# Kernel tuning notes

Hardware: AMD Instinct MI355X
Metric: run time of the kernel (lower is better)

## Reference

```python
import jax, jax.numpy as jnp
import numpy as np

H = 12
D_K = 64
NEG = -1e9
EPS = 1e-6
SQRT_2_PI = float(np.sqrt(2.0 / np.pi))


def gelu_tanh(x):
    return 0.5 * x * (1.0 + jnp.tanh(SQRT_2_PI * (x + 0.044715 * x * x * x)))


def layernorm(x, a, b):
    # torch std is unbiased (ddof=1); note original adds eps to std, not var
    mean = jnp.mean(x, axis=-1, keepdims=True)
    n = x.shape[-1]
    var = jnp.sum((x - mean) ** 2, axis=-1, keepdims=True) / (n - 1)
    std = jnp.sqrt(var)
    return a * (x - mean) / (std + EPS) + b


def setup_inputs() -> dict:
    key = jax.random.key(0)
    ks = jax.random.split(key, 16)
    B, S, D, F = 8, 1024, 768, 3072
    s = 0.02
    inp = {
        "x": jax.random.normal(ks[0], (B, S, D), jnp.float32),
        "mask": jnp.ones((B, 1, 1, S), jnp.int32),
        "Wq": jax.random.normal(ks[1], (D, D), jnp.float32) * s,
        "bq": jnp.zeros((D,), jnp.float32),
        "Wk": jax.random.normal(ks[2], (D, D), jnp.float32) * s,
        "bk": jnp.zeros((D,), jnp.float32),
        "Wv": jax.random.normal(ks[3], (D, D), jnp.float32) * s,
        "bv": jnp.zeros((D,), jnp.float32),
        "Wo": jax.random.normal(ks[4], (D, D), jnp.float32) * s,
        "bo": jnp.zeros((D,), jnp.float32),
        "W1": jax.random.normal(ks[5], (D, F), jnp.float32) * s,
        "b1": jnp.zeros((F,), jnp.float32),
        "W2": jax.random.normal(ks[6], (F, D), jnp.float32) * s,
        "b2": jnp.zeros((D,), jnp.float32),
        "ln1_a": jnp.ones((D,), jnp.float32),
        "ln1_b": jnp.ones((D,), jnp.float32),
        "ln2_a": jnp.ones((D,), jnp.float32),
        "ln2_b": jnp.ones((D,), jnp.float32),
    }
    return inp


def reference(x, mask, Wq, bq, Wk, bk, Wv, bv, Wo, bo, W1, b1, W2, b2,
              ln1_a, ln1_b, ln2_a, ln2_b):
    B, S, D = x.shape
    # QKV projections -> [B, H, S, d_k]
    def split_heads(t):
        return t.reshape(B, S, H, D_K).transpose(0, 2, 1, 3)
    q = split_heads(x @ Wq + bq)
    k = split_heads(x @ Wk + bk)
    v = split_heads(x @ Wv + bv)
    scores = jnp.einsum("bhqd,bhkd->bhqk", q, k) / jnp.sqrt(jnp.float32(D_K))
    scores = jnp.where(mask == 0, jnp.float32(NEG), scores)
    p = jax.nn.softmax(scores, axis=-1)
    attn = jnp.einsum("bhqk,bhkd->bhqd", p, v)
    attn = attn.transpose(0, 2, 1, 3).reshape(B, S, D)
    attn_out = attn @ Wo + bo
    out1 = layernorm(x + attn_out, ln1_a, ln1_b)
    ffn = gelu_tanh(out1 @ W1 + b1) @ W2 + b2
    out2 = layernorm(out1 + ffn, ln2_a, ln2_b)
    return out2
```

## Files before the change

kernel.cpp:

```cpp
#include <hip/hip_runtime.h>
#include <hip/hip_bf16.h>
#include <math.h>

#define BB 8
#define SS 1024
#define DD 768
#define FF 3072
#define HH 12
#define DK 64

typedef __bf16 bf16;
typedef __attribute__((ext_vector_type(8))) __bf16 bf16x8;
typedef __attribute__((ext_vector_type(4))) __bf16 bf16x4;
typedef __attribute__((ext_vector_type(4))) float f32x4;

#define AS1 __attribute__((address_space(1)))
#define AS3 __attribute__((address_space(3)))

#define EXP2_SCALE 0.18033688011112042f
#define NLOG2E2    -2.8853900817779268f

__device__ __forceinline__ float gelu_fast(float x) {
    const float u = 0.7978845608028654f * (x + 0.044715f * x * x * x);
    const float e = __builtin_amdgcn_exp2f(u * NLOG2E2);
    return x * __builtin_amdgcn_rcpf(1.0f + e);
}

template<int BN, int OUTB, int GELU_F, int RESID>
__global__ __launch_bounds__(256) void gemm_bf16(
    const bf16* __restrict__ A, const bf16* __restrict__ Bt,
    const float* __restrict__ bias, const float* __restrict__ R,
    void* __restrict__ Cout, int M, int N, int K)
{
    constexpr int NTJ   = BN / 32;
    constexpr int BITER = (BN * 8) / 256;

    __shared__ bf16x8 As[1024];
    __shared__ bf16x8 Bs[BN * 8];

    const int t    = threadIdx.x;
    const int wave = t >> 6;
    const int lane = t & 63;
    const int mtiles = M >> 7;
    const int m0 = (blockIdx.x % mtiles) * 128;
    const int n0 = (blockIdx.x / mtiles) * BN;
    const int wm = (wave >> 1) * 64;
    const int wn = (wave & 1) * (BN / 2);
    const int col  = lane & 15;
    const int quad = lane >> 4;

    f32x4 acc[4][NTJ] = {};

    const bf16* Abase = A  + (size_t)m0 * K;
    const bf16* Bbase = Bt + (size_t)n0 * K;

    for (int k0 = 0; k0 < K; k0 += 64) {
        if (k0) __syncthreads();

        #pragma unroll
        for (int i = 0; i < 4; ++i) {
            const int chunk = i * 256 + wave * 64 + lane;
            const int r  = chunk >> 3;
            const int kc = (chunk & 7) ^ (r & 7);
            const bf16* ga = Abase + (size_t)r * K + k0 + kc * 8;
            __builtin_amdgcn_global_load_lds((AS1 void*)ga, (AS3 void*)(As + i * 256 + wave * 64), 16, 0, 0);
        }
        #pragma unroll
        for (int i = 0; i < BITER; ++i) {
            const int chunk = i * 256 + wave * 64 + lane;
            const int r  = chunk >> 3;
            const int kc = (chunk & 7) ^ (r & 7);
            const bf16* gb = Bbase + (size_t)r * K + k0 + kc * 8;
            __builtin_amdgcn_global_load_lds((AS1 void*)gb, (AS3 void*)(Bs + i * 256 + wave * 64), 16, 0, 0);
        }
        __syncthreads();

        const bf16* Asp = (const bf16*)As;
        const bf16* Bsp = (const bf16*)Bs;
        #pragma unroll
        for (int ks = 0; ks < 2; ++ks) {
            bf16x8 af[4], bfr[NTJ];
            #pragma unroll
            for (int ti = 0; ti < 4; ++ti) {
                const int r  = wm + ti * 16 + col;
                const int cs = (ks * 4 + quad) ^ (r & 7);
                af[ti] = *(const bf16x8*)(Asp + r * 64 + cs * 8);
            }
            #pragma unroll
            for (int tj = 0; tj < NTJ; ++tj) {
                const int r  = wn + tj * 16 + col;
                const int cs = (ks * 4 + quad) ^ (r & 7);
                bfr[tj] = *(const bf16x8*)(Bsp + r * 64 + cs * 8);
            }
            #pragma unroll
            for (int ti = 0; ti < 4; ++ti)
                #pragma unroll
                for (int tj = 0; tj < NTJ; ++tj)
                    acc[ti][tj] = __builtin_amdgcn_mfma_f32_16x16x32_bf16(
                        af[ti], bfr[tj], acc[ti][tj], 0, 0, 0);
        }
    }

    float biasv[NTJ];
    #pragma unroll
    for (int tj = 0; tj < NTJ; ++tj) biasv[tj] = bias[n0 + wn + tj * 16 + col];

    #pragma unroll
    for (int ti = 0; ti < 4; ++ti) {
        #pragma unroll
        for (int tj = 0; tj < NTJ; ++tj) {
            const int n = n0 + wn + tj * 16 + col;
            #pragma unroll
            for (int i = 0; i < 4; ++i) {
                const int m = m0 + wm + ti * 16 + quad * 4 + i;
                float v = acc[ti][tj][i] + biasv[tj];
                if (GELU_F) v = gelu_fast(v);
                if (RESID) v += R[(size_t)m * N + n];
                if (OUTB) ((bf16*)Cout)[(size_t)m * N + n] = (bf16)v;
                else      ((float*)Cout)[(size_t)m * N + n] = v;
            }
        }
    }
}

__device__ __forceinline__ void tc32(
    const float* __restrict__ src, bf16* __restrict__ dst,
    int R, int C, int c0, int r0, int t)
{
    __shared__ float tile[32][33];
    const int tx = t & 31, ty = t >> 5;
    #pragma unroll
    for (int i = 0; i < 32; i += 8)
        tile[ty + i][tx] = src[(size_t)(r0 + ty + i) * C + c0 + tx];
    __syncthreads();
    #pragma unroll
    for (int i = 0; i < 32; i += 8)
        dst[(size_t)(c0 + ty + i) * R + r0 + tx] = (bf16)tile[tx][ty + i];
}

__global__ __launch_bounds__(256) void prep_all(
    const float* __restrict__ Wq, const float* __restrict__ Wk,
    const float* __restrict__ Wv, const float* __restrict__ Wo,
    const float* __restrict__ W1, const float* __restrict__ W2,
    const float* __restrict__ bq, const float* __restrict__ bk,
    const float* __restrict__ bv, const float* __restrict__ x,
    bf16* __restrict__ wqkvb, bf16* __restrict__ wob,
    bf16* __restrict__ wt1b,  bf16* __restrict__ wt2b,
    float* __restrict__ bqkv, bf16x4* __restrict__ xb)
{
    const int blk = blockIdx.x;
    const int t = threadIdx.x;
    if (blk < 2304) {
        const int job = blk / 576, loc = blk % 576;
        const int c0 = (loc % 24) * 32, r0 = (loc / 24) * 32;
        const float* src = (job == 0) ? Wq : (job == 1) ? Wk : (job == 2) ? Wv : Wo;
        bf16* dst = (job == 3) ? wob : wqkvb + (size_t)job * DD * DD;
        tc32(src, dst, DD, DD, c0, r0, t);
    } else if (blk < 4608) {
        const int loc = blk - 2304;
        tc32(W1, wt1b, DD, FF, (loc % 96) * 32, (loc / 96) * 32, t);
    } else if (blk < 6912) {
        const int loc = blk - 4608;
        tc32(W2, wt2b, FF, DD, (loc % 24) * 32, (loc / 24) * 32, t);
    } else if (blk < 6921) {
        const int i = (blk - 6912) * 256 + t;
        if (i < 3 * DD)
            bqkv[i] = (i < DD) ? bq[i] : (i < 2 * DD ? bk[i - DD] : bv[i - 2 * DD]);
    } else {
        const int i = (blk - 6921) * 256 + t;
        const float4 v = ((const float4*)x)[i];
        bf16x4 o;
        o.x = (bf16)v.x; o.y = (bf16)v.y; o.z = (bf16)v.z; o.w = (bf16)v.w;
        xb[i] = o;
    }
}

__global__ __launch_bounds__(256) void vtrans(
    const bf16* __restrict__ qkvb, bf16* __restrict__ vtb)
{
    __shared__ bf16 tile[32][33];
    const int s0 = blockIdx.x * 32, d0 = blockIdx.y * 32;
    const int bh = blockIdx.z;
    const int b = bh / HH, h = bh % HH;
    const int tx = threadIdx.x & 31, ty = threadIdx.x >> 5;
    #pragma unroll
    for (int i = 0; i < 32; i += 8)
        tile[ty + i][tx] = qkvb[(size_t)(b * SS + s0 + ty + i) * 2304 + 1536 + h * DK + d0 + tx];
    __syncthreads();
    #pragma unroll
    for (int i = 0; i < 32; i += 8)
        vtb[(size_t)(bh * DK + d0 + ty + i) * SS + s0 + tx] = tile[tx][ty + i];
}

__global__ __launch_bounds__(256) void flash_mfma(
    const bf16* __restrict__ qkvb,
    const bf16* __restrict__ vtb,
    const int*  __restrict__ mask,
    bf16* __restrict__ O)
{
    __shared__ bf16x8 Ks[512];
    __shared__ bf16x8 Vs[512];
    __shared__ bf16   Ps[4 * 32 * 64];

    const int t    = threadIdx.x;
    const int wave = t >> 6;
    const int lane = t & 63;
    const int col  = lane & 15;
    const int quad = lane >> 4;
    const int bh = blockIdx.x % (BB * HH);
    const int q0 = (blockIdx.x / (BB * HH)) * 128;
    const int b  = bh / HH;
    const int h  = bh % HH;

    bf16x8 aq[2][2];
    #pragma unroll
    for (int mi = 0; mi < 2; ++mi)
        #pragma unroll
        for (int ks = 0; ks < 2; ++ks)
            aq[mi][ks] = *(const bf16x8*)(qkvb
                + (size_t)(b * SS + q0 + wave * 32 + mi * 16 + col) * 2304
                + h * DK + ks * 32 + quad * 8);

    f32x4 o[2][4] = {};
    float l_part[2][4] = {};

    bf16* Pw = Ps + wave * 2048;

    for (int c0 = 0; c0 < SS; c0 += 64) {
        if (c0) __syncthreads();

        #pragma unroll
        for (int i = 0; i < 2; ++i) {
            const int s  = i * 256 + wave * 64 + lane;
            const int r  = s >> 3;
            const int kc = (s & 7) ^ (r & 7);
            const bf16* gk = qkvb + (size_t)(b * SS + c0 + r) * 2304 + DD + h * DK + kc * 8;
            __builtin_amdgcn_global_load_lds((AS1 void*)gk, (AS3 void*)(Ks + i * 256 + wave * 64), 16, 0, 0);
            const bf16* gv = vtb + (size_t)(bh * DK + r) * SS + c0 + kc * 8;
            __builtin_amdgcn_global_load_lds((AS1 void*)gv, (AS3 void*)(Vs + i * 256 + wave * 64), 16, 0, 0);
        }
        __syncthreads();

        const bf16* Ksp = (const bf16*)Ks;
        f32x4 s4[2][4] = {};
        {
            bf16x8 kf[2][4];
            #pragma unroll
            for (int ks = 0; ks < 2; ++ks)
                #pragma unroll
                for (int tj = 0; tj < 4; ++tj) {
                    const int r  = tj * 16 + col;
                    const int sl = (ks * 4 + quad) ^ (r & 7);
                    kf[ks][tj] = *(const bf16x8*)(Ksp + r * 64 + sl * 8);
                }
            #pragma unroll
            for (int mi = 0; mi < 2; ++mi)
                #pragma unroll
                for (int ks = 0; ks < 2; ++ks)
                    #pragma unroll
                    for (int tj = 0; tj < 4; ++tj)
                        s4[mi][tj] = __builtin_amdgcn_mfma_f32_16x16x32_bf16(
                            aq[mi][ks], kf[ks][tj], s4[mi][tj], 0, 0, 0);
        }

        int mk[4];
        #pragma unroll
        for (int tj = 0; tj < 4; ++tj) mk[tj] = mask[b * SS + c0 + tj * 16 + col];

        #pragma unroll
        for (int mi = 0; mi < 2; ++mi)
            #pragma unroll
            for (int i = 0; i < 4; ++i) {
                const int rf = mi * 16 + quad * 4 + i;
                #pragma unroll
                for (int tj = 0; tj < 4; ++tj) {
                    const float sv = (mk[tj] == 0) ? -1e9f : s4[mi][tj][i];
                    const float p = __builtin_amdgcn_exp2f(sv * EXP2_SCALE);
                    l_part[mi][i] += p;
                    const int c  = tj * 16 + col;
                    const int sl = ((c >> 3) ^ (rf & 7));
                    Pw[rf * 64 + sl * 8 + (c & 7)] = (bf16)p;
                }
            }

        const bf16* Vsp = (const bf16*)Vs;
        bf16x8 vf[2][4];
        #pragma unroll
        for (int ks = 0; ks < 2; ++ks)
            #pragma unroll
            for (int tj = 0; tj < 4; ++tj) {
                const int r  = tj * 16 + col;
                const int sl = (ks * 4 + quad) ^ (r & 7);
                vf[ks][tj] = *(const bf16x8*)(Vsp + r * 64 + sl * 8);
            }
        #pragma unroll
        for (int mi = 0; mi < 2; ++mi) {
            bf16x8 pf[2];
            #pragma unroll
            for (int ks = 0; ks < 2; ++ks) {
                const int rf = mi * 16 + col;
                const int sl = (ks * 4 + quad) ^ (rf & 7);
                pf[ks] = *(const bf16x8*)(Pw + rf * 64 + sl * 8);
            }
            #pragma unroll
            for (int ks = 0; ks < 2; ++ks)
                #pragma unroll
                for (int tj = 0; tj < 4; ++tj)
                    o[mi][tj] = __builtin_amdgcn_mfma_f32_16x16x32_bf16(
                        pf[ks], vf[ks][tj], o[mi][tj], 0, 0, 0);
        }
    }

    #pragma unroll
    for (int mi = 0; mi < 2; ++mi)
        #pragma unroll
        for (int i = 0; i < 4; ++i) {
            float l = l_part[mi][i];
            #pragma unroll
            for (int off = 1; off < 16; off <<= 1)
                l += __shfl_xor(l, off, 64);
            const float inv = 1.0f / l;
            const int q = q0 + wave * 32 + mi * 16 + quad * 4 + i;
            #pragma unroll
            for (int tj = 0; tj < 4; ++tj)
                O[(size_t)(b * SS + q) * DD + h * DK + tj * 16 + col] =
                    (bf16)(o[mi][tj][i] * inv);
        }
}

__global__ __launch_bounds__(256) void layernorm_k(
    const float* __restrict__ X,
    const float* __restrict__ ga, const float* __restrict__ gb,
    float* __restrict__ out, bf16* __restrict__ outb)
{
    __shared__ float red[4];
    const int row = blockIdx.x;
    const int t   = threadIdx.x;
    const float* x = X + (size_t)row * DD;

    float v[3];
    #pragma unroll
    for (int i = 0; i < 3; ++i) v[i] = x[t + i * 256];

    float s = v[0] + v[1] + v[2];
    #pragma unroll
    for (int off = 32; off > 0; off >>= 1) s += __shfl_down(s, off, 64);
    if ((t & 63) == 0) red[t >> 6] = s;
    __syncthreads();
    const float mean = (red[0] + red[1] + red[2] + red[3]) * (1.0f / 768.0f);
    __syncthreads();

    float sq = 0.f;
    #pragma unroll
    for (int i = 0; i < 3; ++i) { const float d = v[i] - mean; sq += d * d; }
    #pragma unroll
    for (int off = 32; off > 0; off >>= 1) sq += __shfl_down(sq, off, 64);
    if ((t & 63) == 0) red[t >> 6] = sq;
    __syncthreads();
    const float var = (red[0] + red[1] + red[2] + red[3]) * (1.0f / 767.0f);
    const float inv = 1.0f / (sqrtf(var) + 1e-6f);

    #pragma unroll
    for (int i = 0; i < 3; ++i) {
        const int c = t + i * 256;
        const float r = ga[c] * (v[i] - mean) * inv + gb[c];
        out[(size_t)row * DD + c] = r;
        if (outb) outb[(size_t)row * DD + c] = (bf16)r;
    }
}

extern "C" void kernel_launch(void* const* d_in, const int* in_sizes, int n_in,
                              void* d_out, int out_size, void* d_ws, size_t ws_size,
                              hipStream_t stream)
{
    const float* x    = (const float*)d_in[0];
    const int*   mask = (const int*)  d_in[1];
    const float* Wq   = (const float*)d_in[2];
    const float* bq   = (const float*)d_in[3];
    const float* Wk   = (const float*)d_in[4];
    const float* bk   = (const float*)d_in[5];
    const float* Wv   = (const float*)d_in[6];
    const float* bv   = (const float*)d_in[7];
    const float* Wo   = (const float*)d_in[8];
    const float* bo   = (const float*)d_in[9];
    const float* W1   = (const float*)d_in[10];
    const float* b1   = (const float*)d_in[11];
    const float* W2   = (const float*)d_in[12];
    const float* b2   = (const float*)d_in[13];
    const float* ln1a = (const float*)d_in[14];
    const float* ln1b = (const float*)d_in[15];
    const float* ln2a = (const float*)d_in[16];
    const float* ln2b = (const float*)d_in[17];
    float* out = (float*)d_out;

    const int M = BB * SS;
    const size_t nBSD = (size_t)M * DD;

    char* w = (char*)d_ws;
    bf16*  qkvb  = (bf16*)w;            w += (size_t)M * 3 * DD * 2;
    bf16*  vtb   = (bf16*)w;            w += (size_t)BB * HH * DK * SS * 2;
    bf16*  attnb = (bf16*)w;            w += nBSD * 2;
    float* attn_sum = (float*)w;        w += nBSD * 4;
    float* out1  = (float*)w;           w += nBSD * 4;
    float* ffn_sum = (float*)w;         w += nBSD * 4;
    bf16*  xb    = (bf16*)w;            w += nBSD * 2;
    bf16*  hbuf  = (bf16*)w;            w += (size_t)M * FF * 2;
    bf16*  wqkvb = (bf16*)w;            w += (size_t)3 * DD * DD * 2;
    bf16*  wob   = (bf16*)w;            w += (size_t)DD * DD * 2;
    bf16*  wt1b  = (bf16*)w;            w += (size_t)DD * FF * 2;
    bf16*  wt2b  = (bf16*)w;            w += (size_t)FF * DD * 2;
    float* bqkv  = (float*)w;           w += (size_t)3 * DD * 4;
    bf16*  out1b = xb;

    const dim3 blk(256);

    prep_all<<<dim3(13065), blk, 0, stream>>>(
        Wq, Wk, Wv, Wo, W1, W2, bq, bk, bv, x,
        wqkvb, wob, wt1b, wt2b, bqkv, (bf16x4*)xb);

    gemm_bf16<128, 1, 0, 0><<<dim3((M / 128) * (3 * DD / 128)), blk, 0, stream>>>(
        xb, wqkvb, bqkv, nullptr, qkvb, M, 3 * DD, DD);

    vtrans<<<dim3(SS / 32, DK / 32, BB * HH), blk, 0, stream>>>(qkvb, vtb);

    flash_mfma<<<dim3((SS / 128) * BB * HH), blk, 0, stream>>>(qkvb, vtb, mask, attnb);

    gemm_bf16<64, 0, 0, 1><<<dim3((M / 128) * (DD / 64)), blk, 0, stream>>>(
        attnb, wob, bo, x, attn_sum, M, DD, DD);

    layernorm_k<<<dim3(M), blk, 0, stream>>>(attn_sum, ln1a, ln1b, out1, out1b);

    gemm_bf16<128, 1, 1, 0><<<dim3((M / 128) * (FF / 128)), blk, 0, stream>>>(
        out1b, wt1b, b1, nullptr, hbuf, M, FF, DD);

    gemm_bf16<64, 0, 0, 1><<<dim3((M / 128) * (DD / 64)), blk, 0, stream>>>(
        hbuf, wt2b, b2, out1, ffn_sum, M, DD, FF);

    layernorm_k<<<dim3(M), blk, 0, stream>>>(ffn_sum, ln2a, ln2b, out, nullptr);
}
```

Measured before the change: 364.0 us.

## Store residual sums in bf16 and double flash attention key chunk per barrier

The Wo and W2 GEMM outputs (pre-layernorm residual sums) are now written as bf16 instead of fp32. The layernorms read bf16, the first layernorm stops writing its fp32 copy, and the second residual add reads the bf16 out1. Flash attention now loads 128 keys per barrier, processed as two 64-key halves with doubled LDS buffers, and applies the mask as an additive bias folded into an fma. This cuts intermediate memory traffic and barrier count, at the cost of bf16 rounding on residual paths and more LDS per block, which may lower occupancy.

```diff
diff --git a/kernel.cpp b/kernel.cpp
--- a/kernel.cpp
+++ b/kernel.cpp
@@ -19,6 +19,7 @@
 
 #define EXP2_SCALE 0.18033688011112042f
 #define NLOG2E2    -2.8853900817779268f
+#define MASK_BIAS  -1.8e8f
 
 __device__ __forceinline__ float gelu_fast(float x) {
     const float u = 0.7978845608028654f * (x + 0.044715f * x * x * x);
@@ -26,10 +27,10 @@
     return x * __builtin_amdgcn_rcpf(1.0f + e);
 }
 
-template<int BN, int OUTB, int GELU_F, int RESID>
+template<int BN, int OUTB, int GELU_F, int RESID, int RB>
 __global__ __launch_bounds__(256) void gemm_bf16(
     const bf16* __restrict__ A, const bf16* __restrict__ Bt,
-    const float* __restrict__ bias, const float* __restrict__ R,
+    const float* __restrict__ bias, const void* __restrict__ R,
     void* __restrict__ Cout, int M, int N, int K)
 {
     constexpr int NTJ   = BN / 32;
@@ -115,7 +116,11 @@
                 const int m = m0 + wm + ti * 16 + quad * 4 + i;
                 float v = acc[ti][tj][i] + biasv[tj];
                 if (GELU_F) v = gelu_fast(v);
-                if (RESID) v += R[(size_t)m * N + n];
+                if (RESID) {
+                    const size_t idx = (size_t)m * N + n;
+                    v += RB ? (float)((const bf16*)R)[idx]
+                            : ((const float*)R)[idx];
+                }
                 if (OUTB) ((bf16*)Cout)[(size_t)m * N + n] = (bf16)v;
                 else      ((float*)Cout)[(size_t)m * N + n] = v;
             }
@@ -198,8 +203,8 @@
     const int*  __restrict__ mask,
     bf16* __restrict__ O)
 {
-    __shared__ bf16x8 Ks[512];
-    __shared__ bf16x8 Vs[512];
+    __shared__ bf16x8 Ks[1024];
+    __shared__ bf16x8 Vs[1024];
     __shared__ bf16   Ps[4 * 32 * 64];
 
     const int t    = threadIdx.x;
@@ -226,88 +231,105 @@
 
     bf16* Pw = Ps + wave * 2048;
 
-    for (int c0 = 0; c0 < SS; c0 += 64) {
+    for (int c0 = 0; c0 < SS; c0 += 128) {
         if (c0) __syncthreads();
 
         #pragma unroll
-        for (int i = 0; i < 2; ++i) {
-            const int s  = i * 256 + wave * 64 + lane;
-            const int r  = s >> 3;
-            const int kc = (s & 7) ^ (r & 7);
-            const bf16* gk = qkvb + (size_t)(b * SS + c0 + r) * 2304 + DD + h * DK + kc * 8;
-            __builtin_amdgcn_global_load_lds((AS1 void*)gk, (AS3 void*)(Ks + i * 256 + wave * 64), 16, 0, 0);
-            const bf16* gv = vtb + (size_t)(bh * DK + r) * SS + c0 + kc * 8;
-            __builtin_amdgcn_global_load_lds((AS1 void*)gv, (AS3 void*)(Vs + i * 256 + wave * 64), 16, 0, 0);
+        for (int i = 0; i < 4; ++i) {
+            const int chunk = i * 256 + wave * 64 + lane;
+            const int half  = chunk >> 9;
+            const int wi    = chunk & 511;
+            const int r  = wi >> 3;
+            const int kc = (wi & 7) ^ (r & 7);
+            const bf16* gk = qkvb + (size_t)(b * SS + c0 + half * 64 + r) * 2304
+                           + DD + h * DK + kc * 8;
+            __builtin_amdgcn_global_load_lds((AS1 void*)gk, (AS3 void*)(Ks + chunk - lane + lane), 16, 0, 0);
+        }
+        #pragma unroll
+        for (int i = 0; i < 4; ++i) {
+            const int chunk = i * 256 + wave * 64 + lane;
+            const int half  = chunk >> 9;
+            const int wi    = chunk & 511;
+            const int r  = wi >> 3;
+            const int kc = (wi & 7) ^ (r & 7);
+            const bf16* gv = vtb + (size_t)(bh * DK + r) * SS + c0 + half * 64 + kc * 8;
+            __builtin_amdgcn_global_load_lds((AS1 void*)gv, (AS3 void*)(Vs + chunk - lane + lane), 16, 0, 0);
         }
         __syncthreads();
 
-        const bf16* Ksp = (const bf16*)Ks;
-        f32x4 s4[2][4] = {};
-        {
-            bf16x8 kf[2][4];
+        #pragma unroll
+        for (int half = 0; half < 2; ++half) {
+            const bf16* Ksp = (const bf16*)(Ks + half * 512);
+            const bf16* Vsp = (const bf16*)(Vs + half * 512);
+            const int ch0 = c0 + half * 64;
+
+            f32x4 s4[2][4] = {};
+            {
+                bf16x8 kf[2][4];
+                #pragma unroll
+                for (int ks = 0; ks < 2; ++ks)
+                    #pragma unroll
+                    for (int tj = 0; tj < 4; ++tj) {
+                        const int r  = tj * 16 + col;
+                        const int sl = (ks * 4 + quad) ^ (r & 7);
+                        kf[ks][tj] = *(const bf16x8*)(Ksp + r * 64 + sl * 8);
+                    }
+                #pragma unroll
+                for (int mi = 0; mi < 2; ++mi)
+                    #pragma unroll
+                    for (int ks = 0; ks < 2; ++ks)
+                        #pragma unroll
+                        for (int tj = 0; tj < 4; ++tj)
+                            s4[mi][tj] = __builtin_amdgcn_mfma_f32_16x16x32_bf16(
+                                aq[mi][ks], kf[ks][tj], s4[mi][tj], 0, 0, 0);
+            }
+
+            float addb[4];
+            #pragma unroll
+            for (int tj = 0; tj < 4; ++tj)
+                addb[tj] = mask[b * SS + ch0 + tj * 16 + col] ? 0.0f : MASK_BIAS;
+
+            #pragma unroll
+            for (int mi = 0; mi < 2; ++mi)
+                #pragma unroll
+                for (int i = 0; i < 4; ++i) {
+                    const int rf = mi * 16 + quad * 4 + i;
+                    #pragma unroll
+                    for (int tj = 0; tj < 4; ++tj) {
+                        const float p = __builtin_amdgcn_exp2f(
+                            fmaf(s4[mi][tj][i], EXP2_SCALE, addb[tj]));
+                        l_part[mi][i] += p;
+                        const int c  = tj * 16 + col;
+                        const int sl = ((c >> 3) ^ (rf & 7));
+                        Pw[rf * 64 + sl * 8 + (c & 7)] = (bf16)p;
+                    }
+                }
+
+            bf16x8 vf[2][4];
             #pragma unroll
             for (int ks = 0; ks < 2; ++ks)
                 #pragma unroll
                 for (int tj = 0; tj < 4; ++tj) {
                     const int r  = tj * 16 + col;
                     const int sl = (ks * 4 + quad) ^ (r & 7);
-                    kf[ks][tj] = *(const bf16x8*)(Ksp + r * 64 + sl * 8);
+                    vf[ks][tj] = *(const bf16x8*)(Vsp + r * 64 + sl * 8);
                 }
             #pragma unroll
-            for (int mi = 0; mi < 2; ++mi)
+            for (int mi = 0; mi < 2; ++mi) {
+                bf16x8 pf[2];
+                #pragma unroll
+                for (int ks = 0; ks < 2; ++ks) {
+                    const int rf = mi * 16 + col;
+                    const int sl = (ks * 4 + quad) ^ (rf & 7);
+                    pf[ks] = *(const bf16x8*)(Pw + rf * 64 + sl * 8);
+                }
                 #pragma unroll
                 for (int ks = 0; ks < 2; ++ks)
                     #pragma unroll
                     for (int tj = 0; tj < 4; ++tj)
-                        s4[mi][tj] = __builtin_amdgcn_mfma_f32_16x16x32_bf16(
-                            aq[mi][ks], kf[ks][tj], s4[mi][tj], 0, 0, 0);
-        }
-
-        int mk[4];
-        #pragma unroll
-        for (int tj = 0; tj < 4; ++tj) mk[tj] = mask[b * SS + c0 + tj * 16 + col];
-
-        #pragma unroll
-        for (int mi = 0; mi < 2; ++mi)
-            #pragma unroll
-            for (int i = 0; i < 4; ++i) {
-                const int rf = mi * 16 + quad * 4 + i;
-                #pragma unroll
-                for (int tj = 0; tj < 4; ++tj) {
-                    const float sv = (mk[tj] == 0) ? -1e9f : s4[mi][tj][i];
-                    const float p = __builtin_amdgcn_exp2f(sv * EXP2_SCALE);
-                    l_part[mi][i] += p;
-                    const int c  = tj * 16 + col;
-                    const int sl = ((c >> 3) ^ (rf & 7));
-                    Pw[rf * 64 + sl * 8 + (c & 7)] = (bf16)p;
-                }
+                        o[mi][tj] = __builtin_amdgcn_mfma_f32_16x16x32_bf16(
+                            pf[ks], vf[ks][tj], o[mi][tj], 0, 0, 0);
             }
-
-        const bf16* Vsp = (const bf16*)Vs;
-        bf16x8 vf[2][4];
-        #pragma unroll
-        for (int ks = 0; ks < 2; ++ks)
-            #pragma unroll
-            for (int tj = 0; tj < 4; ++tj) {
-                const int r  = tj * 16 + col;
-                const int sl = (ks * 4 + quad) ^ (r & 7);
-                vf[ks][tj] = *(const bf16x8*)(Vsp + r * 64 + sl * 8);
-            }
-        #pragma unroll
-        for (int mi = 0; mi < 2; ++mi) {
-            bf16x8 pf[2];
-            #pragma unroll
-            for (int ks = 0; ks < 2; ++ks) {
-                const int rf = mi * 16 + col;
-                const int sl = (ks * 4 + quad) ^ (rf & 7);
-                pf[ks] = *(const bf16x8*)(Pw + rf * 64 + sl * 8);
-            }
-            #pragma unroll
-            for (int ks = 0; ks < 2; ++ks)
-                #pragma unroll
-                for (int tj = 0; tj < 4; ++tj)
-                    o[mi][tj] = __builtin_amdgcn_mfma_f32_16x16x32_bf16(
-                        pf[ks], vf[ks][tj], o[mi][tj], 0, 0, 0);
         }
     }
 
@@ -329,18 +351,18 @@
 }
 
 __global__ __launch_bounds__(256) void layernorm_k(
-    const float* __restrict__ X,
+    const bf16* __restrict__ X,
     const float* __restrict__ ga, const float* __restrict__ gb,
     float* __restrict__ out, bf16* __restrict__ outb)
 {
     __shared__ float red[4];
     const int row = blockIdx.x;
     const int t   = threadIdx.x;
-    const float* x = X + (size_t)row * DD;
+    const bf16* x = X + (size_t)row * DD;
 
     float v[3];
     #pragma unroll
-    for (int i = 0; i < 3; ++i) v[i] = x[t + i * 256];
+    for (int i = 0; i < 3; ++i) v[i] = (float)x[t + i * 256];
 
     float s = v[0] + v[1] + v[2];
     #pragma unroll
@@ -364,7 +386,7 @@
     for (int i = 0; i < 3; ++i) {
         const int c = t + i * 256;
         const float r = ga[c] * (v[i] - mean) * inv + gb[c];
-        out[(size_t)row * DD + c] = r;
+        if (out)  out[(size_t)row * DD + c] = r;
         if (outb) outb[(size_t)row * DD + c] = (bf16)r;
     }
 }
@@ -400,9 +422,8 @@
     bf16*  qkvb  = (bf16*)w;            w += (size_t)M * 3 * DD * 2;
     bf16*  vtb   = (bf16*)w;            w += (size_t)BB * HH * DK * SS * 2;
     bf16*  attnb = (bf16*)w;            w += nBSD * 2;
-    float* attn_sum = (float*)w;        w += nBSD * 4;
-    float* out1  = (float*)w;           w += nBSD * 4;
-    float* ffn_sum = (float*)w;         w += nBSD * 4;
+    bf16*  attn_sumb = (bf16*)w;        w += nBSD * 2;
+    bf16*  ffn_sumb  = (bf16*)w;        w += nBSD * 2;
     bf16*  xb    = (bf16*)w;            w += nBSD * 2;
     bf16*  hbuf  = (bf16*)w;            w += (size_t)M * FF * 2;
     bf16*  wqkvb = (bf16*)w;            w += (size_t)3 * DD * DD * 2;
@@ -418,23 +439,23 @@
         Wq, Wk, Wv, Wo, W1, W2, bq, bk, bv, x,
         wqkvb, wob, wt1b, wt2b, bqkv, (bf16x4*)xb);
 
-    gemm_bf16<128, 1, 0, 0><<<dim3((M / 128) * (3 * DD / 128)), blk, 0, stream>>>(
+    gemm_bf16<128, 1, 0, 0, 0><<<dim3((M / 128) * (3 * DD / 128)), blk, 0, stream>>>(
         xb, wqkvb, bqkv, nullptr, qkvb, M, 3 * DD, DD);
 
     vtrans<<<dim3(SS / 32, DK / 32, BB * HH), blk, 0, stream>>>(qkvb, vtb);
 
     flash_mfma<<<dim3((SS / 128) * BB * HH), blk, 0, stream>>>(qkvb, vtb, mask, attnb);
 
-    gemm_bf16<64, 0, 0, 1><<<dim3((M / 128) * (DD / 64)), blk, 0, stream>>>(
-        attnb, wob, bo, x, attn_sum, M, DD, DD);
-
-    layernorm_k<<<dim3(M), blk, 0, stream>>>(attn_sum, ln1a, ln1b, out1, out1b);
-
-    gemm_bf16<128, 1, 1, 0><<<dim3((M / 128) * (FF / 128)), blk, 0, stream>>>(
+    gemm_bf16<64, 1, 0, 1, 0><<<dim3((M / 128) * (DD / 64)), blk, 0, stream>>>(
+        attnb, wob, bo, x, attn_sumb, M, DD, DD);
+
+    layernorm_k<<<dim3(M), blk, 0, stream>>>(attn_sumb, ln1a, ln1b, nullptr, out1b);
+
+    gemm_bf16<128, 1, 1, 0, 0><<<dim3((M / 128) * (FF / 128)), blk, 0, stream>>>(
         out1b, wt1b, b1, nullptr, hbuf, M, FF, DD);
 
-    gemm_bf16<64, 0, 0, 1><<<dim3((M / 128) * (DD / 64)), blk, 0, stream>>>(
-        hbuf, wt2b, b2, out1, ffn_sum, M, DD, FF);
-
-    layernorm_k<<<dim3(M), blk, 0, stream>>>(ffn_sum, ln2a, ln2b, out, nullptr);
-}
+    gemm_bf16<64, 1, 0, 1, 1><<<dim3((M / 128) * (DD / 64)), blk, 0, stream>>>(
+        hbuf, wt2b, b2, out1b, ffn_sumb, M, DD, FF);
+
+    layernorm_k<<<dim3(M), blk, 0, stream>>>(ffn_sumb, ln2a, ln2b, out, nullptr);
+}
```

Measured after the change: 376.7 us. 3.5% more time.
